# Kernel tuning notes

Measured on AMD Instinct MI355X. Metric: run time of the kernel, lower is better.

## Reference

```python
import jax, jax.numpy as jnp
import numpy as np

V, E, H, M, B, S = 32000, 512, 1024, 256, 2, 1024
GC = 24  # smear_gate_channels = min(24, embedding_dim)


def setup_inputs() -> dict:
    key = jax.random.key(0)
    ks = jax.random.split(key, 20)
    s = 0.02
    return {
        "input_ids": jax.random.randint(ks[0], (B, S), 0, V),
        "emb": jax.random.normal(ks[1], (V, E)) * s,
        "W_ih": jax.random.normal(ks[2], (3 * H, E)) * s,
        "W_hh": jax.random.normal(ks[3], (3 * H, H)) * s,
        "b_ih": jax.random.normal(ks[4], (3 * H,)) * s,
        "b_hh": jax.random.normal(ks[5], (3 * H,)) * s,
        "Wq": jax.random.normal(ks[6], (M, H)) * s,
        "bq": jax.random.normal(ks[7], (M,)) * s,
        "Wk": jax.random.normal(ks[8], (M, H)) * s,
        "bk": jax.random.normal(ks[9], (M,)) * s,
        "Wg": jax.random.normal(ks[10], (1, H)) * s,
        "bg": jax.random.normal(ks[11], (1,)) * s,
        "Whe": jax.random.normal(ks[12], (E, H)) * s,
        "bhe": jax.random.normal(ks[13], (E,)) * s,
        "out_bias": jax.random.normal(ks[14], (V,)) * s,
        "memory_scale": jnp.float32(6.0),
        "smear_W": jax.random.normal(ks[15], (1, GC)) * s,
        "smear_lambda": jax.random.normal(ks[16], (1,)) * 0.1,
    }


def forward(input_ids, emb, W_ih, W_hh, b_ih, b_hh, Wq, bq, Wk, bk, Wg, bg,
            Whe, bhe, out_bias, memory_scale, smear_W, smear_lambda):
    x = emb[input_ids]  # (B,S,E)
    # smear: gated copy of previous token embedding into current
    sg = smear_lambda * jax.nn.sigmoid(x[:, 1:, :GC] @ smear_W.T)  # (B,S-1,1)
    x = jnp.concatenate([x[:, :1], x[:, 1:] + sg * x[:, :-1]], axis=1)
    # GRU (PyTorch gate order r,z,n); precompute input projections
    xg = x @ W_ih.T + b_ih  # (B,S,3H)

    def step(h, xg_t):
        xr, xz, xn = jnp.split(xg_t, 3, axis=-1)
        hg = h @ W_hh.T + b_hh
        hr, hz, hn = jnp.split(hg, 3, axis=-1)
        r = jax.nn.sigmoid(xr + hr)
        z = jax.nn.sigmoid(xz + hz)
        n = jnp.tanh(xn + r * hn)
        h_new = (1.0 - z) * n + z * h
        return h_new, h_new

    h0 = jnp.zeros((x.shape[0], H), dtype=x.dtype)
    _, states = jax.lax.scan(step, h0, jnp.swapaxes(xg, 0, 1))
    states = jnp.swapaxes(states, 0, 1)  # (B,S,H); dropout is identity at eval
    # tied output projection
    base_logits = (states @ Whe.T + bhe) @ emb.T + out_bias  # (B,S,V)
    q = states @ Wq.T + bq  # (B,S,M)
    k = states @ Wk.T + bk
    scores = jnp.einsum("bsm,btm->bst", q, k) / jnp.sqrt(jnp.float32(M))
    mask = jnp.tril(jnp.ones((S, S), dtype=bool), k=-1)[None]  # (1,S,S)
    scores = jnp.where(mask, scores, jnp.finfo(scores.dtype).min)
    attn = jax.nn.softmax(scores, axis=-1) * mask
    attn = attn / jnp.maximum(attn.sum(axis=-1, keepdims=True), 1e-6)
    g = jax.nn.sigmoid(states @ Wg.T + bg)  # (B,S,1)
    gated = attn * (g * memory_scale)  # (B,S,S)
    # scatter_add gated attention into vocab logits at input_ids positions
    b_idx = jnp.arange(B)[:, None, None]
    s_idx = jnp.arange(S)[None, :, None]
    v_idx = input_ids[:, None, :]  # broadcasts to (B,S,S)
    base_logits = base_logits.at[b_idx, s_idx, v_idx].add(gated)
    return base_logits


def reference(input_ids, emb, W_ih, W_hh, b_ih, b_hh, Wq, bq, Wk, bk, Wg, bg,
              Whe, bhe, out_bias, memory_scale, smear_W, smear_lambda):
    return forward(input_ids, emb, W_ih, W_hh, b_ih, b_hh, Wq, bq, Wk, bk,
                   Wg, bg, Whe, bhe, out_bias, memory_scale, smear_W, smear_lambda)
```

## Files before the change

### kernel.cpp

```cpp
#include <hip/hip_runtime.h>
#include <stdint.h>

#define V_ 32000
#define E_ 512
#define H_ 1024
#define M_ 256
#define B_ 2
#define S_ 1024
#define GC_ 24

typedef unsigned short u16;
typedef unsigned int u32;
typedef unsigned long long u64;

typedef __attribute__((ext_vector_type(8))) short short8;
typedef __attribute__((ext_vector_type(4))) float floatx4;
typedef __attribute__((ext_vector_type(2))) float floatx2;
typedef __attribute__((ext_vector_type(2))) _Float16 halfx2;

__device__ __forceinline__ float bf2f(u16 u){ return __uint_as_float(((u32)u) << 16); }
__device__ __forceinline__ float bflo(u32 u){ return __uint_as_float(u << 16); }
__device__ __forceinline__ float bfhi(u32 u){ return __uint_as_float(u & 0xffff0000u); }
__device__ __forceinline__ u16 f2bf(float f){
  u32 u = __float_as_uint(f);
  u32 r = (u + 0x7fffu + ((u >> 16) & 1u)) >> 16;
  return (u16)r;
}
__device__ __forceinline__ float sigm(float x){ return 1.f / (1.f + __expf(-x)); }

__device__ __forceinline__ float dot2f16(u32 a, u32 b, float c){
#if __has_builtin(__builtin_amdgcn_fdot2)
  return __builtin_amdgcn_fdot2(__builtin_bit_cast(halfx2, a),
                                __builtin_bit_cast(halfx2, b), c, false);
#else
  halfx2 av = __builtin_bit_cast(halfx2, a);
  halfx2 bv = __builtin_bit_cast(halfx2, b);
  return fmaf((float)av.y, (float)bv.y, fmaf((float)av.x, (float)bv.x, c));
#endif
}

__global__ __launch_bounds__(64) void detect_kernel(const u32* __restrict__ emb,
    int* __restrict__ flag, float* __restrict__ scal,
    const void* __restrict__ lam, const void* __restrict__ ms)
{
  int lane = threadIdx.x;
  int c = 0;
  for (int i = lane; i < 256; i += 64){
    u32 w = emb[i];
    float a = fabsf(__uint_as_float((w & 0xffffu) << 16));
    if (a > 1e-5f && a < 1.0f) c++;
  }
  #pragma unroll
  for (int o = 32; o; o >>= 1) c += __shfl_down(c, o, 64);
  if (lane == 0){
    int isf32 = (c < 128) ? 1 : 0;
    *flag = isf32;
    if (isf32) scal[0] = ((const float*)lam)[0];
    else {
      float v = bf2f(((const u16*)lam)[0]);
      scal[0] = (fabsf(v) <= 4.0f) ? v : ((const float*)lam)[0];
    }
    if (isf32) scal[1] = ((const float*)ms)[0];
    else {
      u16 a = ((const u16*)ms)[0];
      float v = bf2f(a);
      scal[1] = (a != 0 && fabsf(v) > 1e-4f && fabsf(v) < 1e4f) ? v : ((const float*)ms)[0];
    }
  }
}

__global__ __launch_bounds__(256) void conv_kernel(const void* __restrict__ src,
    u16* __restrict__ dst, int n, const int* __restrict__ flag)
{
  int i = blockIdx.x * 256 + threadIdx.x;
  if (i >= n) return;
  if (*flag) dst[i] = f2bf(((const float*)src)[i]);
  else       dst[i] = ((const u16*)src)[i];
}

__global__ __launch_bounds__(256) void convh_kernel(const void* __restrict__ src,
    u16* __restrict__ dst, int n, const int* __restrict__ flag)
{
  int i = blockIdx.x * 256 + threadIdx.x;
  if (i >= n) return;
  float v = (*flag) ? ((const float*)src)[i] : bf2f(((const u16*)src)[i]);
  _Float16 h = (_Float16)v;
  dst[i] = __builtin_bit_cast(u16, h);
}

__global__ __launch_bounds__(64) void smear_kernel(const int* __restrict__ ids,
    const u16* __restrict__ emb, const u16* __restrict__ smW,
    const float* __restrict__ scal, u16* __restrict__ xs)
{
  int row = blockIdx.x;
  int t = row & (S_ - 1);
  int lane = threadIdx.x;
  int id = ids[row];
  const u16* er = emb + (size_t)id * E_;
  float sg = 0.f;
  if (t > 0){
    float p = 0.f;
    if (lane < GC_) p = bf2f(er[lane]) * bf2f(smW[lane]);
    #pragma unroll
    for (int o = 32; o; o >>= 1) p += __shfl_down(p, o, 64);
    float dot = __shfl(p, 0, 64);
    sg = scal[0] * sigm(dot);
  }
  uint4 cur = ((const uint4*)er)[lane];
  uint4 outv = cur;
  if (t > 0){
    const u16* ep = emb + (size_t)ids[row - 1] * E_;
    uint4 prv = ((const uint4*)ep)[lane];
    const u16* cu = (const u16*)&cur;
    const u16* pu = (const u16*)&prv;
    u16* po = (u16*)&outv;
    #pragma unroll
    for (int j = 0; j < 8; j++) po[j] = f2bf(bf2f(cu[j]) + sg * bf2f(pu[j]));
  }
  ((uint4*)(xs + (size_t)row * E_))[lane] = outv;
}

template<bool OUT_BF16>
__global__ __launch_bounds__(256) void gemm_bt(
    const u16* __restrict__ A, const u16* __restrict__ Bm,
    const u16* __restrict__ bias, void* __restrict__ Cout,
    int K, int Ndim)
{
  int wave = threadIdx.x >> 6, lane = threadIdx.x & 63;
  int wm = wave >> 1, wn = wave & 1;
  int m0 = blockIdx.y * 128 + wm * 64;
  int n0 = blockIdx.x * 128 + wn * 64;
  int lrow = lane & 15, lq = lane >> 4;
  floatx4 acc[4][4];
  #pragma unroll
  for (int i = 0; i < 4; i++)
    #pragma unroll
    for (int j = 0; j < 4; j++) acc[i][j] = (floatx4)0.f;
  const u16* Ab = A + (size_t)(m0 + lrow) * K + lq * 8;
  const u16* Bb = Bm + (size_t)(n0 + lrow) * K + lq * 8;
  for (int k0 = 0; k0 < K; k0 += 32){
    short8 af[4], bfr[4];
    #pragma unroll
    for (int tt = 0; tt < 4; tt++)
      af[tt] = *(const short8*)(Ab + (size_t)tt * 16 * K + k0);
    #pragma unroll
    for (int tt = 0; tt < 4; tt++)
      bfr[tt] = *(const short8*)(Bb + (size_t)tt * 16 * K + k0);
    #pragma unroll
    for (int im = 0; im < 4; im++)
      #pragma unroll
      for (int in = 0; in < 4; in++)
        acc[im][in] = __builtin_amdgcn_mfma_f32_16x16x32_bf16(af[im], bfr[in], acc[im][in], 0, 0, 0);
  }
  #pragma unroll
  for (int in = 0; in < 4; in++){
    int n = n0 + in * 16 + lrow;
    float bv = bf2f(bias[n]);
    #pragma unroll
    for (int im = 0; im < 4; im++){
      int mb = m0 + im * 16 + lq * 4;
      #pragma unroll
      for (int r = 0; r < 4; r++){
        float v = acc[im][in][r] + bv;
        size_t off = (size_t)(mb + r) * Ndim + n;
        if (OUT_BF16) ((u16*)Cout)[off] = f2bf(v);
        else          ((float*)Cout)[off] = v;
      }
    }
  }
}

__global__ __launch_bounds__(1024) void gru_kernel(
    const float* __restrict__ xg, const u16* __restrict__ W_hh,
    const u16* __restrict__ b_hh, u64* __restrict__ hslot,
    u16* __restrict__ states)
{
  const int b = blockIdx.x >> 5;
  const int ibase = (blockIdx.x & 31) * 32;
  const int tid = threadIdx.x;
  const int kg = tid >> 5;
  const int il = tid & 31;
  const int i = ibase + il;
  const int w = tid >> 6;

  __shared__ float lds_h[2][H_];
  __shared__ u32   lds_hpk[2][H_ / 2];
  __shared__ float lds_xg[2][96];
  __shared__ float red[3][16][32];

  uint4 Wv[3][4];
  #pragma unroll
  for (int g = 0; g < 3; g++){
    const uint4* p = (const uint4*)(W_hh + ((size_t)(g * H_ + i)) * H_ + kg * 32);
    #pragma unroll
    for (int q = 0; q < 4; q++) Wv[g][q] = p[q];
  }
  float bh0 = bf2f(b_hh[i]);
  float bh1 = bf2f(b_hh[H_ + i]);
  float bh2 = bf2f(b_hh[2 * H_ + i]);

  float xg_next = 0.f;
  if (tid < 96)
    xg_next = xg[((size_t)(b * S_)) * 3072 + (tid >> 5) * H_ + ibase + (tid & 31)];

  for (int t = 0; t < S_; t++){
    const int cur = t & 1;
    if (tid < 512){
      const u64* rptr = hslot + ((size_t)((cur ^ 1) * B_ + b)) * H_ + 2 * tid;
      u64 u0, u1;
      do {
        u0 = __hip_atomic_load(rptr,     __ATOMIC_RELAXED, __HIP_MEMORY_SCOPE_AGENT);
        u1 = __hip_atomic_load(rptr + 1, __ATOMIC_RELAXED, __HIP_MEMORY_SCOPE_AGENT);
      } while (((u32)(u0 >> 32) != (u32)t) || ((u32)(u1 >> 32) != (u32)t));
      float h0 = __uint_as_float((u32)u0);
      float h1 = __uint_as_float((u32)u1);
      *(floatx2*)&lds_h[cur][2 * tid] = (floatx2){h0, h1};
      lds_hpk[cur][tid] = __builtin_bit_cast(u32, __builtin_amdgcn_cvt_pkrtz(h0, h1));
    }
    if (tid < 96) lds_xg[cur][tid] = xg_next;
    __syncthreads();
    if (tid < 96 && t + 1 < S_)
      xg_next = xg[((size_t)(b * S_ + t + 1)) * 3072 + (tid >> 5) * H_ + ibase + (tid & 31)];

    const u32* hp = &lds_hpk[cur][kg * 16];
    float pr = 0.f, pz = 0.f, pn = 0.f;
    #pragma unroll
    for (int q = 0; q < 4; q++){
      uint4 wr = Wv[0][q], wz = Wv[1][q], wn4 = Wv[2][q];
      u32 cr[4] = {wr.x, wr.y, wr.z, wr.w};
      u32 cz[4] = {wz.x, wz.y, wz.z, wz.w};
      u32 cn[4] = {wn4.x, wn4.y, wn4.z, wn4.w};
      #pragma unroll
      for (int e = 0; e < 4; e++){
        u32 h2 = hp[q * 4 + e];
        pr = dot2f16(cr[e], h2, pr);
        pz = dot2f16(cz[e], h2, pz);
        pn = dot2f16(cn[e], h2, pn);
      }
    }
    pr += __shfl_xor(pr, 32, 64);
    pz += __shfl_xor(pz, 32, 64);
    pn += __shfl_xor(pn, 32, 64);
    if ((tid & 63) < 32){
      red[0][w][il] = pr; red[1][w][il] = pz; red[2][w][il] = pn;
    }
    __syncthreads();
    if (tid < 32){
      __builtin_amdgcn_s_setprio(3);
      float hr = 0.f, hz = 0.f, hn = 0.f;
      #pragma unroll
      for (int ww = 0; ww < 16; ww++){
        hr += red[0][ww][tid]; hz += red[1][ww][tid]; hn += red[2][ww][tid];
      }
      float r = sigm(lds_xg[cur][tid] + hr + bh0);
      float z = sigm(lds_xg[cur][32 + tid] + hz + bh1);
      float xx = lds_xg[cur][64 + tid] + r * (hn + bh2);
      float ax = fabsf(xx);
      float et = __expf(-2.f * ax);
      float n = copysignf((1.f - et) * __builtin_amdgcn_rcpf(1.f + et), xx);
      float ho = lds_h[cur][ibase + tid];
      float hnew = (1.f - z) * n + z * ho;
      u64 pk = (((u64)(u32)(t + 1)) << 32) | (u64)__float_as_uint(hnew);
      __hip_atomic_store(hslot + ((size_t)(cur * B_ + b)) * H_ + ibase + tid, pk,
                         __ATOMIC_RELAXED, __HIP_MEMORY_SCOPE_AGENT);
      states[((size_t)(b * S_ + t)) * H_ + ibase + tid] = f2bf(hnew);
      __builtin_amdgcn_s_setprio(0);
    }
  }
}

__global__ __launch_bounds__(256) void gk_kernel(const u16* __restrict__ states,
    const u16* __restrict__ Wg, const u16* __restrict__ bg, float* __restrict__ gws)
{
  int row = blockIdx.x * 4 + (threadIdx.x >> 6);
  int lane = threadIdx.x & 63;
  const u16* sr = states + (size_t)row * H_;
  float p = 0.f;
  #pragma unroll
  for (int j = 0; j < 16; j++){
    int c = j * 64 + lane;
    p += bf2f(sr[c]) * bf2f(Wg[c]);
  }
  #pragma unroll
  for (int o = 32; o; o >>= 1) p += __shfl_xor(p, o, 64);
  if (lane == 0) gws[row] = sigm(p + bf2f(bg[0]));
}

__global__ __launch_bounds__(1024) void sort_kernel(const int* __restrict__ ids, int* __restrict__ sorted)
{
  int b = blockIdx.x, tid = threadIdx.x;
  __shared__ int arr[S_];
  arr[tid] = (ids[b * S_ + tid] << 11) | tid;
  __syncthreads();
  for (int k = 2; k <= S_; k <<= 1){
    for (int j = k >> 1; j > 0; j >>= 1){
      int ixj = tid ^ j;
      if (ixj > tid){
        int a = arr[tid], c = arr[ixj];
        bool dir = (tid & k) == 0;
        if (dir ? (a > c) : (a < c)){ arr[tid] = c; arr[ixj] = a; }
      }
      __syncthreads();
    }
  }
  sorted[b * S_ + tid] = arr[tid];
}

__global__ __launch_bounds__(256) void attn_kernel(
    const u16* __restrict__ q, const u16* __restrict__ k,
    const float* __restrict__ gws, const float* __restrict__ scal,
    float* __restrict__ gated)
{
  int s = blockIdx.x, b = blockIdx.y;
  if (s == 0) return;
  int tid = threadIdx.x;
  __shared__ float qs[M_];
  __shared__ float rbm[4], rbs[4];
  if (tid < M_) qs[tid] = bf2f(q[((size_t)(b * S_ + s)) * M_ + tid]);
  __syncthreads();
  float myS[4];
  float lmax = -1e30f;
  #pragma unroll
  for (int r = 0; r < 4; r++){
    int t = tid + 256 * r;
    if (t < s){
      const uint4* kr = (const uint4*)(k + ((size_t)(b * S_ + t)) * M_);
      float d = 0.f;
      #pragma unroll
      for (int j = 0; j < 32; j++){
        uint4 kv = kr[j];
        u32 cc[4] = {kv.x, kv.y, kv.z, kv.w};
        #pragma unroll
        for (int e = 0; e < 4; e++)
          d += bflo(cc[e]) * qs[j * 8 + e * 2] + bfhi(cc[e]) * qs[j * 8 + e * 2 + 1];
      }
      d *= 0.0625f;
      myS[r] = d;
      lmax = fmaxf(lmax, d);
    }
  }
  #pragma unroll
  for (int o = 32; o; o >>= 1) lmax = fmaxf(lmax, __shfl_xor(lmax, o, 64));
  if ((tid & 63) == 0) rbm[tid >> 6] = lmax;
  __syncthreads();
  float gmax = fmaxf(fmaxf(rbm[0], rbm[1]), fmaxf(rbm[2], rbm[3]));
  float lsum = 0.f;
  #pragma unroll
  for (int r = 0; r < 4; r++){
    int t = tid + 256 * r;
    if (t < s){ myS[r] = __expf(myS[r] - gmax); lsum += myS[r]; }
  }
  #pragma unroll
  for (int o = 32; o; o >>= 1) lsum += __shfl_xor(lsum, o, 64);
  if ((tid & 63) == 0) rbs[tid >> 6] = lsum;
  __syncthreads();
  float gsum = rbs[0] + rbs[1] + rbs[2] + rbs[3];
  float fac = gws[b * S_ + s] * scal[1] / gsum;
  float* grow = gated + ((size_t)(b * S_ + s)) * S_;
  #pragma unroll
  for (int r = 0; r < 4; r++){
    int t = tid + 256 * r;
    if (t < s) grow[t] = myS[r] * fac;
  }
}

__global__ __launch_bounds__(256) void scatter_kernel(
    const int* __restrict__ sorted, const float* __restrict__ gated,
    float* __restrict__ out)
{
  int gid = blockIdx.x * 256 + threadIdx.x;
  int e = gid & (S_ - 1);
  int row = gid >> 10;
  int s = row & (S_ - 1);
  int b = row >> 10;
  const int* sb = sorted + b * S_;
  int pk = sb[e];
  int v = pk >> 11;
  if (e > 0 && (sb[e - 1] >> 11) == v) return;
  const float* grow = gated + (size_t)row * S_;
  float sum = 0.f; bool any = false;
  for (int j = e; j < S_; j++){
    int pj = sb[j];
    if ((pj >> 11) != v) break;
    int t = pj & 2047;
    if (t < s){ sum += grow[t]; any = true; }
  }
  if (any){
    size_t off = (size_t)row * V_ + v;
    out[off] += sum;
  }
}

extern "C" void kernel_launch(void* const* d_in, const int* in_sizes, int n_in,
                              void* d_out, int out_size, void* d_ws, size_t ws_size,
                              hipStream_t stream)
{
  const int*  ids   = (const int*)d_in[0];
  const void* emb   = d_in[1];
  const void* W_ih  = d_in[2];
  const void* W_hh  = d_in[3];
  const void* b_ih  = d_in[4];
  const void* b_hh  = d_in[5];
  const void* Wq    = d_in[6];
  const void* bq    = d_in[7];
  const void* Wk    = d_in[8];
  const void* bk    = d_in[9];
  const void* Wg    = d_in[10];
  const void* bg    = d_in[11];
  const void* Whe   = d_in[12];
  const void* bhe   = d_in[13];
  const void* obias = d_in[14];
  const void* ms    = d_in[15];
  const void* smW   = d_in[16];
  const void* lam   = d_in[17];
  (void)in_sizes; (void)n_in; (void)out_size; (void)ws_size;

  char* ws = (char*)d_ws;
  int*   flag   = (int*)(ws + 0);
  float* scal   = (float*)(ws + 256);
  u64*   hslot  = (u64*)(ws + 512);
  u16*   c_emb  = (u16*)(ws + 33280);
  u16*   c_Wih  = (u16*)(ws + 32801280);
  u16*   c_Whh  = (u16*)(ws + 35947008);
  u16*   c_Wq   = (u16*)(ws + 42238464);
  u16*   c_Wk   = (u16*)(ws + 42762752);
  u16*   c_Wg   = (u16*)(ws + 43287040);
  u16*   c_Whe  = (u16*)(ws + 43289088);
  u16*   c_bih  = (u16*)(ws + 44337664);
  u16*   c_bhh  = (u16*)(ws + 44343808);
  u16*   c_bq   = (u16*)(ws + 44349952);
  u16*   c_bk   = (u16*)(ws + 44350464);
  u16*   c_bg   = (u16*)(ws + 44350976);
  u16*   c_bhe  = (u16*)(ws + 44351232);
  u16*   c_ob   = (u16*)(ws + 44352256);
  u16*   c_smW  = (u16*)(ws + 44416512);
  u16*   xs     = (u16*)(ws + 44416768);
  float* xg     = (float*)(ws + 46513920);
  u16*   states = (u16*)(ws + 71679744);
  u16*   hs     = (u16*)(ws + 75874048);
  u16*   qb     = (u16*)(ws + 77971200);
  u16*   kb     = (u16*)(ws + 79019776);
  float* gws    = (float*)(ws + 80068352);
  float* gated  = (float*)(ws + 80076544);
  int*   sorted = (int*)(ws + 88465152);
  float* out = (float*)d_out;

  hipMemsetAsync(hslot, 0, 32768, stream);
  detect_kernel<<<dim3(1), dim3(64), 0, stream>>>((const u32*)emb, flag, scal, lam, ms);

  #define CONV(src, dst, n) conv_kernel<<<dim3(((n)+255)/256), dim3(256), 0, stream>>>(src, dst, n, flag)
  CONV(emb,   c_emb, V_ * E_);
  CONV(W_ih,  c_Wih, 3 * H_ * E_);
  convh_kernel<<<dim3((3 * H_ * H_ + 255) / 256), dim3(256), 0, stream>>>(W_hh, c_Whh, 3 * H_ * H_, flag);
  CONV(Wq,    c_Wq,  M_ * H_);
  CONV(Wk,    c_Wk,  M_ * H_);
  CONV(Wg,    c_Wg,  H_);
  CONV(Whe,   c_Whe, E_ * H_);
  CONV(b_ih,  c_bih, 3 * H_);
  CONV(b_hh,  c_bhh, 3 * H_);
  CONV(bq,    c_bq,  M_);
  CONV(bk,    c_bk,  M_);
  CONV(bg,    c_bg,  1);
  CONV(bhe,   c_bhe, E_);
  CONV(obias, c_ob,  V_);
  CONV(smW,   c_smW, GC_);
  #undef CONV

  smear_kernel<<<dim3(B_ * S_), dim3(64), 0, stream>>>(ids, c_emb, c_smW, scal, xs);
  gemm_bt<false><<<dim3(3072 / 128, 2048 / 128), dim3(256), 0, stream>>>(xs, c_Wih, c_bih, (void*)xg, E_, 3072);
  gru_kernel<<<dim3(64), dim3(1024), 0, stream>>>(xg, c_Whh, c_bhh, hslot, states);
  gemm_bt<true><<<dim3(512 / 128, 16), dim3(256), 0, stream>>>(states, c_Whe, c_bhe, (void*)hs, H_, 512);
  gemm_bt<true><<<dim3(256 / 128, 16), dim3(256), 0, stream>>>(states, c_Wq, c_bq, (void*)qb, H_, 256);
  gemm_bt<true><<<dim3(256 / 128, 16), dim3(256), 0, stream>>>(states, c_Wk, c_bk, (void*)kb, H_, 256);
  gk_kernel<<<dim3(512), dim3(256), 0, stream>>>(states, c_Wg, c_bg, gws);
  sort_kernel<<<dim3(B_), dim3(1024), 0, stream>>>(ids, sorted);
  attn_kernel<<<dim3(S_, B_), dim3(256), 0, stream>>>(qb, kb, gws, scal, gated);
  gemm_bt<false><<<dim3(V_ / 128, 16), dim3(256), 0, stream>>>(hs, c_emb, c_ob, (void*)out, E_, V_);
  scatter_kernel<<<dim3(B_ * S_ * S_ / 256), dim3(256), 0, stream>>>(sorted, gated, out);
}
```

Before: 2.822 ms.

## Restructure GRU step so each half-wave owns one output with shuffle reduction

```diff
diff --git a/kernel.cpp b/kernel.cpp
--- a/kernel.cpp
+++ b/kernel.cpp
@@ -178,30 +178,31 @@
   const int b = blockIdx.x >> 5;
   const int ibase = (blockIdx.x & 31) * 32;
   const int tid = threadIdx.x;
-  const int kg = tid >> 5;
-  const int il = tid & 31;
-  const int i = ibase + il;
   const int w = tid >> 6;
-
-  __shared__ float lds_h[2][H_];
+  const int l = tid & 63;
+  const int half = l >> 5;
+  const int kl = l & 31;
+  const int ol = 2 * w + half;
+  const int i = ibase + ol;
+
   __shared__ u32   lds_hpk[2][H_ / 2];
   __shared__ float lds_xg[2][96];
-  __shared__ float red[3][16][32];
 
   uint4 Wv[3][4];
   #pragma unroll
   for (int g = 0; g < 3; g++){
-    const uint4* p = (const uint4*)(W_hh + ((size_t)(g * H_ + i)) * H_ + kg * 32);
+    const uint4* p = (const uint4*)(W_hh + ((size_t)(g * H_ + i)) * H_ + kl * 32);
     #pragma unroll
     for (int q = 0; q < 4; q++) Wv[g][q] = p[q];
   }
   float bh0 = bf2f(b_hh[i]);
   float bh1 = bf2f(b_hh[H_ + i]);
   float bh2 = bf2f(b_hh[2 * H_ + i]);
+  float ho = 0.f;
 
   float xg_next = 0.f;
   if (tid < 96)
-    xg_next = xg[((size_t)(b * S_)) * 3072 + (tid >> 5) * H_ + ibase + (tid & 31)];
+    xg_next = xg[((size_t)(b * S_)) * 3072 + (tid >> 5) * 1024 + ibase + (tid & 31)];
 
   for (int t = 0; t < S_; t++){
     const int cur = t & 1;
@@ -212,17 +213,15 @@
         u0 = __hip_atomic_load(rptr,     __ATOMIC_RELAXED, __HIP_MEMORY_SCOPE_AGENT);
         u1 = __hip_atomic_load(rptr + 1, __ATOMIC_RELAXED, __HIP_MEMORY_SCOPE_AGENT);
       } while (((u32)(u0 >> 32) != (u32)t) || ((u32)(u1 >> 32) != (u32)t));
-      float h0 = __uint_as_float((u32)u0);
-      float h1 = __uint_as_float((u32)u1);
-      *(floatx2*)&lds_h[cur][2 * tid] = (floatx2){h0, h1};
-      lds_hpk[cur][tid] = __builtin_bit_cast(u32, __builtin_amdgcn_cvt_pkrtz(h0, h1));
+      lds_hpk[cur][tid] = __builtin_bit_cast(u32, __builtin_amdgcn_cvt_pkrtz(
+          __uint_as_float((u32)u0), __uint_as_float((u32)u1)));
     }
     if (tid < 96) lds_xg[cur][tid] = xg_next;
     __syncthreads();
     if (tid < 96 && t + 1 < S_)
-      xg_next = xg[((size_t)(b * S_ + t + 1)) * 3072 + (tid >> 5) * H_ + ibase + (tid & 31)];
-
-    const u32* hp = &lds_hpk[cur][kg * 16];
+      xg_next = xg[((size_t)(b * S_ + t + 1)) * 3072 + (tid >> 5) * 1024 + ibase + (tid & 31)];
+
+    const u32* hp = &lds_hpk[cur][kl * 16];
     float pr = 0.f, pz = 0.f, pn = 0.f;
     #pragma unroll
     for (int q = 0; q < 4; q++){
@@ -238,34 +237,27 @@
         pn = dot2f16(cn[e], h2, pn);
       }
     }
-    pr += __shfl_xor(pr, 32, 64);
-    pz += __shfl_xor(pz, 32, 64);
-    pn += __shfl_xor(pn, 32, 64);
-    if ((tid & 63) < 32){
-      red[0][w][il] = pr; red[1][w][il] = pz; red[2][w][il] = pn;
+    #pragma unroll
+    for (int o = 1; o < 32; o <<= 1){
+      pr += __shfl_xor(pr, o, 64);
+      pz += __shfl_xor(pz, o, 64);
+      pn += __shfl_xor(pn, o, 64);
+    }
+    float r = sigm(lds_xg[cur][ol] + pr + bh0);
+    float z = sigm(lds_xg[cur][32 + ol] + pz + bh1);
+    float xx = lds_xg[cur][64 + ol] + r * (pn + bh2);
+    float ax = fabsf(xx);
+    float et = __expf(-2.f * ax);
+    float n = copysignf((1.f - et) * __builtin_amdgcn_rcpf(1.f + et), xx);
+    float hnew = (1.f - z) * n + z * ho;
+    ho = hnew;
+    if (kl == 0){
+      u64 pk = (((u64)(u32)(t + 1)) << 32) | (u64)__float_as_uint(hnew);
+      __hip_atomic_store(hslot + ((size_t)(cur * B_ + b)) * H_ + i, pk,
+                         __ATOMIC_RELAXED, __HIP_MEMORY_SCOPE_AGENT);
+      states[((size_t)(b * S_ + t)) * H_ + i] = f2bf(hnew);
     }
     __syncthreads();
-    if (tid < 32){
-      __builtin_amdgcn_s_setprio(3);
-      float hr = 0.f, hz = 0.f, hn = 0.f;
-      #pragma unroll
-      for (int ww = 0; ww < 16; ww++){
-        hr += red[0][ww][tid]; hz += red[1][ww][tid]; hn += red[2][ww][tid];
-      }
-      float r = sigm(lds_xg[cur][tid] + hr + bh0);
-      float z = sigm(lds_xg[cur][32 + tid] + hz + bh1);
-      float xx = lds_xg[cur][64 + tid] + r * (hn + bh2);
-      float ax = fabsf(xx);
-      float et = __expf(-2.f * ax);
-      float n = copysignf((1.f - et) * __builtin_amdgcn_rcpf(1.f + et), xx);
-      float ho = lds_h[cur][ibase + tid];
-      float hnew = (1.f - z) * n + z * ho;
-      u64 pk = (((u64)(u32)(t + 1)) << 32) | (u64)__float_as_uint(hnew);
-      __hip_atomic_store(hslot + ((size_t)(cur * B_ + b)) * H_ + ibase + tid, pk,
-                         __ATOMIC_RELAXED, __HIP_MEMORY_SCOPE_AGENT);
-      states[((size_t)(b * S_ + t)) * H_ + ibase + tid] = f2bf(hnew);
-      __builtin_amdgcn_s_setprio(0);
-    }
   }
 }
 
```

After: 3.605 ms. 27.8% more time.

## Restructure GRU step sync with per-slice LDS flags and packed fp16 hidden slots

Applied to the files above, without the earlier changes.

```diff
diff --git a/kernel.cpp b/kernel.cpp
--- a/kernel.cpp
+++ b/kernel.cpp
@@ -172,7 +172,7 @@
 
 __global__ __launch_bounds__(1024) void gru_kernel(
     const float* __restrict__ xg, const u16* __restrict__ W_hh,
-    const u16* __restrict__ b_hh, u64* __restrict__ hslot,
+    const u16* __restrict__ b_hh, u32* __restrict__ hslot,
     u16* __restrict__ states)
 {
   const int b = blockIdx.x >> 5;
@@ -181,12 +181,10 @@
   const int kg = tid >> 5;
   const int il = tid & 31;
   const int i = ibase + il;
-  const int w = tid >> 6;
-
-  __shared__ float lds_h[2][H_];
+
   __shared__ u32   lds_hpk[2][H_ / 2];
-  __shared__ float lds_xg[2][96];
-  __shared__ float red[3][16][32];
+  __shared__ u32   lds_flag[2][256];
+  __shared__ float lds_acc[2][3][32];
 
   uint4 Wv[3][4];
   #pragma unroll
@@ -195,34 +193,50 @@
     #pragma unroll
     for (int q = 0; q < 4; q++) Wv[g][q] = p[q];
   }
-  float bh0 = bf2f(b_hh[i]);
-  float bh1 = bf2f(b_hh[H_ + i]);
-  float bh2 = bf2f(b_hh[2 * H_ + i]);
-
-  float xg_next = 0.f;
-  if (tid < 96)
-    xg_next = xg[((size_t)(b * S_)) * 3072 + (tid >> 5) * H_ + ibase + (tid & 31)];
+
+  float ho = 0.f, xr0 = 0.f, xz0 = 0.f, xn0 = 0.f, bh0 = 0.f, bh1 = 0.f, bh2 = 0.f;
+  if (tid < 32){
+    bh0 = bf2f(b_hh[ibase + tid]);
+    bh1 = bf2f(b_hh[H_ + ibase + tid]);
+    bh2 = bf2f(b_hh[2 * H_ + ibase + tid]);
+    size_t base = ((size_t)(b * S_)) * 3072 + ibase + tid;
+    xr0 = xg[base]; xz0 = xg[base + 1024]; xn0 = xg[base + 2048];
+  }
+  if (tid < 256){ lds_flag[0][tid] = 0; lds_flag[1][tid] = 0; }
+  if (tid < 192) ((float*)lds_acc)[tid] = 0.f;
+  __syncthreads();
 
   for (int t = 0; t < S_; t++){
-    const int cur = t & 1;
-    if (tid < 512){
-      const u64* rptr = hslot + ((size_t)((cur ^ 1) * B_ + b)) * H_ + 2 * tid;
+    const int p = t & 1;
+    if (tid >= 256 && tid < 512){
+      const int j = tid - 256;
+      const u64* rp = (const u64*)(hslot + ((size_t)((p ^ 1) * B_ + b)) * H_) + 2 * j;
+      const u32 tg = (u32)t;
       u64 u0, u1;
       do {
-        u0 = __hip_atomic_load(rptr,     __ATOMIC_RELAXED, __HIP_MEMORY_SCOPE_AGENT);
-        u1 = __hip_atomic_load(rptr + 1, __ATOMIC_RELAXED, __HIP_MEMORY_SCOPE_AGENT);
-      } while (((u32)(u0 >> 32) != (u32)t) || ((u32)(u1 >> 32) != (u32)t));
-      float h0 = __uint_as_float((u32)u0);
-      float h1 = __uint_as_float((u32)u1);
-      *(floatx2*)&lds_h[cur][2 * tid] = (floatx2){h0, h1};
-      lds_hpk[cur][tid] = __builtin_bit_cast(u32, __builtin_amdgcn_cvt_pkrtz(h0, h1));
-    }
-    if (tid < 96) lds_xg[cur][tid] = xg_next;
-    __syncthreads();
-    if (tid < 96 && t + 1 < S_)
-      xg_next = xg[((size_t)(b * S_ + t + 1)) * 3072 + (tid >> 5) * H_ + ibase + (tid & 31)];
-
-    const u32* hp = &lds_hpk[cur][kg * 16];
+        u0 = __hip_atomic_load(rp,     __ATOMIC_RELAXED, __HIP_MEMORY_SCOPE_AGENT);
+        u1 = __hip_atomic_load(rp + 1, __ATOMIC_RELAXED, __HIP_MEMORY_SCOPE_AGENT);
+      } while ((((u32)(u0 >> 16) & 0xffffu) != tg) | (((u32)(u0 >> 48)) != tg) |
+               (((u32)(u1 >> 16) & 0xffffu) != tg) | (((u32)(u1 >> 48)) != tg));
+      u32 pair0 = ((u32)u0 & 0xffffu) | (((u32)(u0 >> 32)) << 16);
+      u32 pair1 = ((u32)u1 & 0xffffu) | (((u32)(u1 >> 32)) << 16);
+      *(u64*)&lds_hpk[p][2 * j] = (u64)pair0 | ((u64)pair1 << 32);
+      __hip_atomic_store(&lds_flag[p][j], (u32)(t + 1),
+                         __ATOMIC_RELEASE, __HIP_MEMORY_SCOPE_WORKGROUP);
+    }
+    {
+      const u32 want = (u32)(t + 1);
+      const u32* f = &lds_flag[p][kg * 8];
+      for (;;){
+        u32 ok = 1;
+        #pragma unroll
+        for (int j = 0; j < 8; j++)
+          ok &= (__hip_atomic_load(f + j, __ATOMIC_RELAXED,
+                                   __HIP_MEMORY_SCOPE_WORKGROUP) == want) ? 1u : 0u;
+        if (ok) break;
+      }
+    }
+    const u32* hp = &lds_hpk[p][kg * 16];
     float pr = 0.f, pz = 0.f, pn = 0.f;
     #pragma unroll
     for (int q = 0; q < 4; q++){
@@ -242,29 +256,36 @@
     pz += __shfl_xor(pz, 32, 64);
     pn += __shfl_xor(pn, 32, 64);
     if ((tid & 63) < 32){
-      red[0][w][il] = pr; red[1][w][il] = pz; red[2][w][il] = pn;
+      atomicAdd(&lds_acc[p][0][il], pr);
+      atomicAdd(&lds_acc[p][1][il], pz);
+      atomicAdd(&lds_acc[p][2][il], pn);
     }
     __syncthreads();
     if (tid < 32){
-      __builtin_amdgcn_s_setprio(3);
-      float hr = 0.f, hz = 0.f, hn = 0.f;
-      #pragma unroll
-      for (int ww = 0; ww < 16; ww++){
-        hr += red[0][ww][tid]; hz += red[1][ww][tid]; hn += red[2][ww][tid];
-      }
-      float r = sigm(lds_xg[cur][tid] + hr + bh0);
-      float z = sigm(lds_xg[cur][32 + tid] + hz + bh1);
-      float xx = lds_xg[cur][64 + tid] + r * (hn + bh2);
+      float hr = lds_acc[p][0][tid];
+      float hz = lds_acc[p][1][tid];
+      float hn = lds_acc[p][2][tid];
+      float r = sigm(xr0 + hr + bh0);
+      float z = sigm(xz0 + hz + bh1);
+      float xx = xn0 + r * (hn + bh2);
       float ax = fabsf(xx);
       float et = __expf(-2.f * ax);
       float n = copysignf((1.f - et) * __builtin_amdgcn_rcpf(1.f + et), xx);
-      float ho = lds_h[cur][ibase + tid];
       float hnew = (1.f - z) * n + z * ho;
-      u64 pk = (((u64)(u32)(t + 1)) << 32) | (u64)__float_as_uint(hnew);
-      __hip_atomic_store(hslot + ((size_t)(cur * B_ + b)) * H_ + ibase + tid, pk,
+      ho = hnew;
+      lds_acc[p][0][tid] = 0.f;
+      lds_acc[p][1][tid] = 0.f;
+      lds_acc[p][2][tid] = 0.f;
+      asm volatile("s_waitcnt lgkmcnt(0)" ::: "memory");
+      u16 h16 = __builtin_bit_cast(u16, (_Float16)hnew);
+      u32 tgv = (((u32)(t + 1)) << 16) | (u32)h16;
+      __hip_atomic_store(&hslot[((size_t)(p * B_ + b)) * H_ + ibase + tid], tgv,
                          __ATOMIC_RELAXED, __HIP_MEMORY_SCOPE_AGENT);
       states[((size_t)(b * S_ + t)) * H_ + ibase + tid] = f2bf(hnew);
-      __builtin_amdgcn_s_setprio(0);
+      if (t + 1 < S_){
+        size_t base = ((size_t)(b * S_ + t + 1)) * 3072 + ibase + tid;
+        xr0 = xg[base]; xz0 = xg[base + 1024]; xn0 = xg[base + 2048];
+      }
     }
   }
 }
@@ -418,7 +439,7 @@
   char* ws = (char*)d_ws;
   int*   flag   = (int*)(ws + 0);
   float* scal   = (float*)(ws + 256);
-  u64*   hslot  = (u64*)(ws + 512);
+  u32*   hslot  = (u32*)(ws + 512);
   u16*   c_emb  = (u16*)(ws + 33280);
   u16*   c_Wih  = (u16*)(ws + 32801280);
   u16*   c_Whh  = (u16*)(ws + 35947008);
@@ -445,7 +466,7 @@
   int*   sorted = (int*)(ws + 88465152);
   float* out = (float*)d_out;
 
-  hipMemsetAsync(hslot, 0, 32768, stream);
+  hipMemsetAsync(hslot, 0, 16384, stream);
   detect_kernel<<<dim3(1), dim3(64), 0, stream>>>((const u32*)emb, flag, scal, lam, ms);
 
   #define CONV(src, dst, n) conv_kernel<<<dim3(((n)+255)/256), dim3(256), 0, stream>>>(src, dst, n, flag)
```

New measurement: 4.508 ms. 1.6x slower.
